# Performance work log

Hardware: AMD Instinct MI355X
Metric: run time of the kernel (lower is better)

## Reference

```python
import jax, jax.numpy as jnp
import numpy as np

N_V, N_E = 4096, 8192
ATOM_DIM, BOND_DIM_P1, H, N_LAYER = 64, 32, 128, 4


def _leaky(x):
    return jax.nn.leaky_relu(x, negative_slope=0.01)


def setup_inputs() -> dict:
    key = jax.random.key(0)
    ks = jax.random.split(key, 16)
    atom_ftr = jax.random.normal(ks[0], (N_V, ATOM_DIM), dtype=jnp.float32)
    bond_ftr = jax.random.normal(ks[1], (N_E, BOND_DIM_P1), dtype=jnp.float32)
    # one-hot incidence matrices: each edge column selects one source / one dest node
    src = jax.random.randint(ks[2], (N_E,), 0, N_V)
    dst = jax.random.randint(ks[3], (N_E,), 0, N_V)
    vew1 = jnp.zeros((N_V, N_E), jnp.float32).at[src, jnp.arange(N_E)].set(1.0)
    vew2 = jnp.zeros((N_V, N_E), jnp.float32).at[dst, jnp.arange(N_E)].set(1.0)
    def lin(k, o, i):
        s = 1.0 / np.sqrt(i)
        k1, k2 = jax.random.split(k)
        return (jax.random.uniform(k1, (o, i), jnp.float32, -s, s),
                jax.random.uniform(k2, (o,), jnp.float32, -s, s))
    vW1, vb1 = lin(ks[4], H, ATOM_DIM)
    vW2, vb2 = lin(ks[5], H, H)
    eW1, eb1 = lin(ks[6], H, BOND_DIM_P1)
    eW2, eb2 = lin(ks[7], H, H)
    mWs, mbs = [], []
    for l in range(N_LAYER):
        W, b = lin(ks[8 + l], H, H)
        mWs.append(W); mbs.append(b)
    return {
        'atom_ftr': atom_ftr, 'bond_ftr': bond_ftr, 'vew1': vew1, 'vew2': vew2,
        'vW1': vW1, 'vb1': vb1, 'vW2': vW2, 'vb2': vb2,
        'eW1': eW1, 'eb1': eb1, 'eW2': eW2, 'eb2': eb2,
        'mlp_W': jnp.stack(mWs), 'mlp_b': jnp.stack(mbs),
    }


def reference(atom_ftr, bond_ftr, vew1, vew2, vW1, vb1, vW2, vb2,
              eW1, eb1, eW2, eb2, mlp_W, mlp_b):
    # v_linear / e_linear: Linear -> leaky_relu -> Linear -> tanh (dropout p=0)
    hv = jnp.tanh(_leaky(atom_ftr @ vW1.T + vb1) @ vW2.T + vb2)   # [n_v, h]
    he = jnp.tanh(_leaky(bond_ftr @ eW1.T + eb1) @ eW2.T + eb2)   # [n_e, h]
    n_layer = mlp_W.shape[0]
    for l in range(n_layer):
        he_hv_2 = jax.nn.relu(he + vew2.T @ hv)       # [n_e, h]
        hv = hv + vew1 @ he_hv_2                      # [n_v, h]
        hv = _leaky(hv @ mlp_W[l].T + mlp_b[l])       # per-layer MLP (1 linear + leaky_relu)
    he_out = jnp.concatenate([vew1.T @ hv, vew2.T @ hv, he], axis=1)  # [n_e, 3h]
    return hv, he_out
```

## Files before the change

### kernel.cpp

```cpp
#include <hip/hip_runtime.h>
#include <hip/hip_bf16.h>

#define NV 4096
#define NE 8192
#define AD 64
#define BD 32
#define HD 128
#define NL 4
#define DEGCAP 32


__device__ __forceinline__ float leaky(float x) { return x > 0.f ? x : 0.01f * x; }
__device__ __forceinline__ int clampv(int x) { return min(max(x, 0), NV - 1); }

#define W_VW1T 0
#define W_VW2T 8192
#define W_EW1T 24576
#define W_EW2T 28672
#define W_MWT  45056
#define W_VB1  110592
#define W_VB2  110720
#define W_EB1  110848
#define W_EB2  110976
#define W_MB   111104
#define W_TOTAL 111616

#define OUT_HE 524288
#define ESTR   384

#define WS_SRC 0
#define WS_DST 32768
#define WS_DEG 65536
#define WS_ADJ 81920
#define WS_WB  606208
#define WS_HVA 1052672
#define WS_HVB 3149824

__global__ void prep_k(const float* __restrict__ vW1, const float* __restrict__ vW2,
                       const float* __restrict__ eW1, const float* __restrict__ eW2,
                       const float* __restrict__ mW,
                       const float* __restrict__ vb1, const float* __restrict__ vb2,
                       const float* __restrict__ eb1, const float* __restrict__ eb2,
                       const float* __restrict__ mb, float* __restrict__ wb,
                       int* __restrict__ deg) {
    int blk = blockIdx.x, t = threadIdx.x;
    if (blk < 436) {
        int i = blk * 256 + t;
        if (i >= W_TOTAL) return;
        float v;
        if (i < W_VW2T)      { int q = i;          int k = q / 128, j = q % 128; v = vW1[(long)j * AD + k]; }
        else if (i < W_EW1T) { int q = i - W_VW2T; int k = q / 128, j = q % 128; v = vW2[(long)j * HD + k]; }
        else if (i < W_EW2T) { int q = i - W_EW1T; int k = q / 128, j = q % 128; v = eW1[(long)j * BD + k]; }
        else if (i < W_MWT)  { int q = i - W_EW2T; int k = q / 128, j = q % 128; v = eW2[(long)j * HD + k]; }
        else if (i < W_VB1)  { int q = i - W_MWT;  int l = q / 16384, r = q % 16384;
                               int k = r / 128, j = r % 128;
                               v = mW[(long)l * 16384 + (long)j * HD + k]; }
        else if (i < W_VB2)  v = vb1[i - W_VB1];
        else if (i < W_EB1)  v = vb2[i - W_VB2];
        else if (i < W_EB2)  v = eb1[i - W_EB1];
        else if (i < W_MB)   v = eb2[i - W_EB2];
        else                 v = mb[i - W_MB];
        wb[i] = v;
    } else {
        int i = (blk - 436) * 256 + t;
        if (i < NV) deg[i] = 0;
    }
}

template<int K>
__device__ __forceinline__ float4 gemm_row(const float* __restrict__ xrow,
                                           const float* __restrict__ Wt, int jg) {
    float4 c = make_float4(0.f, 0.f, 0.f, 0.f);
    const float4* W4 = (const float4*)Wt;
#pragma unroll 8
    for (int k = 0; k < K; k += 4) {
        float4 xv = *(const float4*)(xrow + k);
        float4 w0 = W4[(k + 0) * 32 + jg];
        float4 w1 = W4[(k + 1) * 32 + jg];
        float4 w2 = W4[(k + 2) * 32 + jg];
        float4 w3 = W4[(k + 3) * 32 + jg];
        c.x = fmaf(xv.x, w0.x, fmaf(xv.y, w1.x, fmaf(xv.z, w2.x, fmaf(xv.w, w3.x, c.x))));
        c.y = fmaf(xv.x, w0.y, fmaf(xv.y, w1.y, fmaf(xv.z, w2.y, fmaf(xv.w, w3.y, c.y))));
        c.z = fmaf(xv.x, w0.z, fmaf(xv.y, w1.z, fmaf(xv.z, w2.z, fmaf(xv.w, w3.z, c.z))));
        c.w = fmaf(xv.x, w0.w, fmaf(xv.y, w1.w, fmaf(xv.z, w2.w, fmaf(xv.w, w3.w, c.w))));
    }
    return c;
}

__global__ __launch_bounds__(256, 3)
void fused_k(const uint4* __restrict__ vew1, const uint4* __restrict__ vew2,
             int* __restrict__ srcv, int* __restrict__ dstv,
             int* __restrict__ deg, int* __restrict__ adj,
             const float* __restrict__ atom, const float* __restrict__ bond,
             const float* __restrict__ wb,
             float* __restrict__ hv, float* __restrict__ outf) {
    __shared__ __align__(16) float xs[8 * AD];
    __shared__ __align__(16) float t1[8 * HD];
    int g = blockIdx.x, t = threadIdx.x;
    int grp = g / 7, rem = g % 7;
    if (rem < 4) {
        int blk = grp * 4 + rem;
        bool isv1 = (blk < 1024);
        const uint4* m = isv1 ? vew1 : vew2;
        int* out = isv1 ? srcv : dstv;
        int r0 = (blk & 1023) * 4;
        const uint4* p = m + (long)r0 * 2048;
#pragma unroll
        for (int b = 0; b < 2; b++) {
            uint4 u[16];
            unsigned o[16];
            int base = b * 4096 + t;
#pragma unroll
            for (int k = 0; k < 16; k++) u[k] = p[base + k * 256];
#pragma unroll
            for (int k = 0; k < 16; k++) o[k] = u[k].x | u[k].y | u[k].z | u[k].w;
            unsigned any = 0;
#pragma unroll
            for (int k = 0; k < 16; k++) any |= o[k];
            if (any == 0u) continue;
#pragma unroll
            for (int k = 0; k < 16; k++) {
                if (o[k] == 0u) continue;
                int i = base + k * 256;
                int row = r0 + (i >> 11);
                int col = (i << 2) & (NE - 1);
#pragma unroll
                for (int q = 0; q < 4; q++) {
                    unsigned val = (q == 0) ? u[k].x : (q == 1) ? u[k].y
                                 : (q == 2) ? u[k].z : u[k].w;
                    if (val) {
                        int e = col + q;
                        out[e] = row;
                        if (isv1) {
                            int pp = atomicAdd(&deg[row], 1);
                            if (pp < DEGCAP) adj[row * DEGCAP + pp] = e;
                        }
                    }
                }
            }
        }
    } else {
        int mu = grp * 3 + (rem - 4);
        int jg = t & 31, rg = t >> 5, j0 = jg * 4;
        if (mu < 512) {
            int r0 = mu * 8;
            for (int i = t; i < 8 * AD; i += 256) xs[i] = atom[(long)r0 * AD + i];
            __syncthreads();
            float4 c1 = gemm_row<AD>(xs + rg * AD, wb + W_VW1T, jg);
            float4 b1 = *(const float4*)(wb + W_VB1 + j0);
            c1.x = leaky(c1.x + b1.x); c1.y = leaky(c1.y + b1.y);
            c1.z = leaky(c1.z + b1.z); c1.w = leaky(c1.w + b1.w);
            *(float4*)(t1 + rg * HD + j0) = c1;
            __syncthreads();
            float4 c2 = gemm_row<HD>(t1 + rg * HD, wb + W_VW2T, jg);
            float4 b2 = *(const float4*)(wb + W_VB2 + j0);
            c2.x = tanhf(c2.x + b2.x); c2.y = tanhf(c2.y + b2.y);
            c2.z = tanhf(c2.z + b2.z); c2.w = tanhf(c2.w + b2.w);
            *(float4*)(hv + (long)(r0 + rg) * HD + j0) = c2;
        } else {
            int r0 = (mu - 512) * 8;
            if (t < 8 * BD) xs[t] = bond[(long)r0 * BD + t];
            __syncthreads();
            float4 c1 = gemm_row<BD>(xs + rg * BD, wb + W_EW1T, jg);
            float4 b1 = *(const float4*)(wb + W_EB1 + j0);
            c1.x = leaky(c1.x + b1.x); c1.y = leaky(c1.y + b1.y);
            c1.z = leaky(c1.z + b1.z); c1.w = leaky(c1.w + b1.w);
            *(float4*)(t1 + rg * HD + j0) = c1;
            __syncthreads();
            float4 c2 = gemm_row<HD>(t1 + rg * HD, wb + W_EW2T, jg);
            float4 b2 = *(const float4*)(wb + W_EB2 + j0);
            c2.x = tanhf(c2.x + b2.x); c2.y = tanhf(c2.y + b2.y);
            c2.z = tanhf(c2.z + b2.z); c2.w = tanhf(c2.w + b2.w);
            *(float4*)(outf + (long)OUT_HE + (long)(r0 + rg) * ESTR + 2 * HD + j0) = c2;
        }
    }
}

__global__ void layer_k(const float* __restrict__ hvin, const float* __restrict__ wb,
                        const int* __restrict__ deg, const int* __restrict__ adj,
                        const int* __restrict__ dstv, const float* __restrict__ outf,
                        float* __restrict__ hvout, int l, float* hv_out) {
    __shared__ __align__(16) float xs[4 * HD];
    int t = threadIdx.x, jg = t & 31, rg = t >> 5, j0 = jg * 4;
    int r = blockIdx.x * 4 + rg;
    float4 x = *(const float4*)(hvin + (long)r * HD + j0);
    int dn = min(deg[r], DEGCAP);
    const int* al = adj + r * DEGCAP;
    for (int i = 0; i < dn; i++) {
        int e = al[i]; e = max(0, min(e, NE - 1));
        int d = clampv(dstv[e]);
        float4 he = *(const float4*)(outf + (long)OUT_HE + (long)e * ESTR + 2 * HD + j0);
        float4 hd = *(const float4*)(hvin + (long)d * HD + j0);
        float s0 = he.x + hd.x, s1 = he.y + hd.y;
        float s2 = he.z + hd.z, s3 = he.w + hd.w;
        x.x += s0 > 0.f ? s0 : 0.f; x.y += s1 > 0.f ? s1 : 0.f;
        x.z += s2 > 0.f ? s2 : 0.f; x.w += s3 > 0.f ? s3 : 0.f;
    }
    *(float4*)(xs + rg * HD + j0) = x;
    __syncthreads();
    float4 c = gemm_row<HD>(xs + rg * HD, wb + W_MWT + l * 16384, jg);
    float4 b = *(const float4*)(wb + W_MB + l * HD + j0);
    c.x = leaky(c.x + b.x); c.y = leaky(c.y + b.y);
    c.z = leaky(c.z + b.z); c.w = leaky(c.w + b.w);
    long o = (long)r * HD + j0;
    *(float4*)(hvout + o) = c;
    if (hv_out) *(float4*)(hv_out + o) = c;
}

__global__ void out_he_k(const float* __restrict__ hv,
                         const int* __restrict__ src, const int* __restrict__ dst,
                         float* __restrict__ outf) {
    int e = blockIdx.x, t = threadIdx.x, j0 = t * 2;
    int s = clampv(src[e]), d = clampv(dst[e]);
    float2 a = *(const float2*)(hv + (long)s * HD + j0);
    float2 b = *(const float2*)(hv + (long)d * HD + j0);
    float* base = outf + (long)OUT_HE + (long)e * ESTR;
    *(float2*)(base + j0) = a;
    *(float2*)(base + HD + j0) = b;
}

extern "C" void kernel_launch(void* const* d_in, const int* in_sizes, int n_in,
                              void* d_out, int out_size, void* d_ws, size_t ws_size,
                              hipStream_t stream) {
    char* ws = (char*)d_ws;
    int*   srcv = (int*)(ws + WS_SRC);
    int*   dstv = (int*)(ws + WS_DST);
    int*   deg  = (int*)(ws + WS_DEG);
    int*   adj  = (int*)(ws + WS_ADJ);
    float* wb   = (float*)(ws + WS_WB);
    float* hvA  = (float*)(ws + WS_HVA);
    float* hvB  = (float*)(ws + WS_HVB);
    float* outf = (float*)d_out;

    prep_k<<<452, 256, 0, stream>>>(
        (const float*)d_in[4], (const float*)d_in[6], (const float*)d_in[8],
        (const float*)d_in[10], (const float*)d_in[12],
        (const float*)d_in[5], (const float*)d_in[7], (const float*)d_in[9],
        (const float*)d_in[11], (const float*)d_in[13], wb, deg);

    fused_k<<<3584, 256, 0, stream>>>(
        (const uint4*)d_in[2], (const uint4*)d_in[3], srcv, dstv, deg, adj,
        (const float*)d_in[0], (const float*)d_in[1], wb, hvA, outf);

    layer_k<<<NV / 4, 128, 0, stream>>>(hvA, wb, deg, adj, dstv, outf, hvB, 0, nullptr);
    layer_k<<<NV / 4, 128, 0, stream>>>(hvB, wb, deg, adj, dstv, outf, hvA, 1, nullptr);
    layer_k<<<NV / 4, 128, 0, stream>>>(hvA, wb, deg, adj, dstv, outf, hvB, 2, nullptr);
    layer_k<<<NV / 4, 128, 0, stream>>>(hvB, wb, deg, adj, dstv, outf, hvA, 3, outf);

    out_he_k<<<NE, 64, 0, stream>>>(hvA, srcv, dstv, outf);
}
```

Before: 410.6 us.

## Build dest adjacency and scatter edge outputs from last layer, use nontemporal loads

Builds a second per-node adjacency list for destination edges during the incidence scan, then has the final layer kernel scatter each node's result directly into the src/dst slices of the edge output. This removes the separate out_he kernel launch and its gather. It also switches the dense incidence matrix reads to nontemporal loads to avoid polluting cache. The cost is extra atomics for vew2 rows and serialized scatter loops per node in the last layer.

```diff
diff --git a/kernel.cpp b/kernel.cpp
--- a/kernel.cpp
+++ b/kernel.cpp
@@ -9,6 +9,8 @@
 #define NL 4
 #define DEGCAP 32
 
+
+typedef unsigned int v4u __attribute__((ext_vector_type(4)));
 
 __device__ __forceinline__ float leaky(float x) { return x > 0.f ? x : 0.01f * x; }
 __device__ __forceinline__ int clampv(int x) { return min(max(x, 0), NV - 1); }
@@ -28,13 +30,15 @@
 #define OUT_HE 524288
 #define ESTR   384
 
-#define WS_SRC 0
-#define WS_DST 32768
-#define WS_DEG 65536
-#define WS_ADJ 81920
-#define WS_WB  606208
-#define WS_HVA 1052672
-#define WS_HVB 3149824
+#define WS_SRC  0
+#define WS_DST  32768
+#define WS_DEGS 65536
+#define WS_ADJS 81920
+#define WS_DEGD 606208
+#define WS_ADJD 622592
+#define WS_WB   1146880
+#define WS_HVA  1593344
+#define WS_HVB  3690496
 
 __global__ void prep_k(const float* __restrict__ vW1, const float* __restrict__ vW2,
                        const float* __restrict__ eW1, const float* __restrict__ eW2,
@@ -42,7 +46,7 @@
                        const float* __restrict__ vb1, const float* __restrict__ vb2,
                        const float* __restrict__ eb1, const float* __restrict__ eb2,
                        const float* __restrict__ mb, float* __restrict__ wb,
-                       int* __restrict__ deg) {
+                       int* __restrict__ degS, int* __restrict__ degD) {
     int blk = blockIdx.x, t = threadIdx.x;
     if (blk < 436) {
         int i = blk * 256 + t;
@@ -63,7 +67,8 @@
         wb[i] = v;
     } else {
         int i = (blk - 436) * 256 + t;
-        if (i < NV) deg[i] = 0;
+        if (i < NV) degS[i] = 0;
+        else if (i < 2 * NV) degD[i - NV] = 0;
     }
 }
 
@@ -88,9 +93,10 @@
 }
 
 __global__ __launch_bounds__(256, 3)
-void fused_k(const uint4* __restrict__ vew1, const uint4* __restrict__ vew2,
+void fused_k(const v4u* __restrict__ vew1, const v4u* __restrict__ vew2,
              int* __restrict__ srcv, int* __restrict__ dstv,
-             int* __restrict__ deg, int* __restrict__ adj,
+             int* __restrict__ degS, int* __restrict__ adjS,
+             int* __restrict__ degD, int* __restrict__ adjD,
              const float* __restrict__ atom, const float* __restrict__ bond,
              const float* __restrict__ wb,
              float* __restrict__ hv, float* __restrict__ outf) {
@@ -101,17 +107,19 @@
     if (rem < 4) {
         int blk = grp * 4 + rem;
         bool isv1 = (blk < 1024);
-        const uint4* m = isv1 ? vew1 : vew2;
+        const v4u* m = isv1 ? vew1 : vew2;
         int* out = isv1 ? srcv : dstv;
+        int* deg = isv1 ? degS : degD;
+        int* adj = isv1 ? adjS : adjD;
         int r0 = (blk & 1023) * 4;
-        const uint4* p = m + (long)r0 * 2048;
+        const v4u* p = m + (long)r0 * 2048;
 #pragma unroll
         for (int b = 0; b < 2; b++) {
-            uint4 u[16];
+            v4u u[16];
             unsigned o[16];
             int base = b * 4096 + t;
 #pragma unroll
-            for (int k = 0; k < 16; k++) u[k] = p[base + k * 256];
+            for (int k = 0; k < 16; k++) u[k] = __builtin_nontemporal_load(&p[base + k * 256]);
 #pragma unroll
             for (int k = 0; k < 16; k++) o[k] = u[k].x | u[k].y | u[k].z | u[k].w;
             unsigned any = 0;
@@ -131,10 +139,8 @@
                     if (val) {
                         int e = col + q;
                         out[e] = row;
-                        if (isv1) {
-                            int pp = atomicAdd(&deg[row], 1);
-                            if (pp < DEGCAP) adj[row * DEGCAP + pp] = e;
-                        }
+                        int pp = atomicAdd(&deg[row], 1);
+                        if (pp < DEGCAP) adj[row * DEGCAP + pp] = e;
                     }
                 }
             }
@@ -177,17 +183,19 @@
 }
 
 __global__ void layer_k(const float* __restrict__ hvin, const float* __restrict__ wb,
-                        const int* __restrict__ deg, const int* __restrict__ adj,
+                        const int* __restrict__ degS, const int* __restrict__ adjS,
+                        const int* __restrict__ degD, const int* __restrict__ adjD,
                         const int* __restrict__ dstv, const float* __restrict__ outf,
-                        float* __restrict__ hvout, int l, float* hv_out) {
+                        float* __restrict__ hvout, int l, float* hv_out,
+                        float* __restrict__ outw) {
     __shared__ __align__(16) float xs[4 * HD];
     int t = threadIdx.x, jg = t & 31, rg = t >> 5, j0 = jg * 4;
     int r = blockIdx.x * 4 + rg;
     float4 x = *(const float4*)(hvin + (long)r * HD + j0);
-    int dn = min(deg[r], DEGCAP);
-    const int* al = adj + r * DEGCAP;
-    for (int i = 0; i < dn; i++) {
-        int e = al[i]; e = max(0, min(e, NE - 1));
+    int dnS = min(degS[r], DEGCAP);
+    const int* alS = adjS + r * DEGCAP;
+    for (int i = 0; i < dnS; i++) {
+        int e = alS[i]; e = max(0, min(e, NE - 1));
         int d = clampv(dstv[e]);
         float4 he = *(const float4*)(outf + (long)OUT_HE + (long)e * ESTR + 2 * HD + j0);
         float4 hd = *(const float4*)(hvin + (long)d * HD + j0);
@@ -204,19 +212,19 @@
     c.z = leaky(c.z + b.z); c.w = leaky(c.w + b.w);
     long o = (long)r * HD + j0;
     *(float4*)(hvout + o) = c;
-    if (hv_out) *(float4*)(hv_out + o) = c;
-}
-
-__global__ void out_he_k(const float* __restrict__ hv,
-                         const int* __restrict__ src, const int* __restrict__ dst,
-                         float* __restrict__ outf) {
-    int e = blockIdx.x, t = threadIdx.x, j0 = t * 2;
-    int s = clampv(src[e]), d = clampv(dst[e]);
-    float2 a = *(const float2*)(hv + (long)s * HD + j0);
-    float2 b = *(const float2*)(hv + (long)d * HD + j0);
-    float* base = outf + (long)OUT_HE + (long)e * ESTR;
-    *(float2*)(base + j0) = a;
-    *(float2*)(base + HD + j0) = b;
+    if (hv_out) {
+        *(float4*)(hv_out + o) = c;
+        for (int i = 0; i < dnS; i++) {
+            int e = alS[i]; e = max(0, min(e, NE - 1));
+            *(float4*)(outw + (long)OUT_HE + (long)e * ESTR + j0) = c;
+        }
+        int dnD = min(degD[r], DEGCAP);
+        const int* alD = adjD + r * DEGCAP;
+        for (int i = 0; i < dnD; i++) {
+            int e = alD[i]; e = max(0, min(e, NE - 1));
+            *(float4*)(outw + (long)OUT_HE + (long)e * ESTR + HD + j0) = c;
+        }
+    }
 }
 
 extern "C" void kernel_launch(void* const* d_in, const int* in_sizes, int n_in,
@@ -225,27 +233,28 @@
     char* ws = (char*)d_ws;
     int*   srcv = (int*)(ws + WS_SRC);
     int*   dstv = (int*)(ws + WS_DST);
-    int*   deg  = (int*)(ws + WS_DEG);
-    int*   adj  = (int*)(ws + WS_ADJ);
+    int*   degS = (int*)(ws + WS_DEGS);
+    int*   adjS = (int*)(ws + WS_ADJS);
+    int*   degD = (int*)(ws + WS_DEGD);
+    int*   adjD = (int*)(ws + WS_ADJD);
     float* wb   = (float*)(ws + WS_WB);
     float* hvA  = (float*)(ws + WS_HVA);
     float* hvB  = (float*)(ws + WS_HVB);
     float* outf = (float*)d_out;
 
-    prep_k<<<452, 256, 0, stream>>>(
+    prep_k<<<468, 256, 0, stream>>>(
         (const float*)d_in[4], (const float*)d_in[6], (const float*)d_in[8],
         (const float*)d_in[10], (const float*)d_in[12],
         (const float*)d_in[5], (const float*)d_in[7], (const float*)d_in[9],
-        (const float*)d_in[11], (const float*)d_in[13], wb, deg);
+        (const float*)d_in[11], (const float*)d_in[13], wb, degS, degD);
 
     fused_k<<<3584, 256, 0, stream>>>(
-        (const uint4*)d_in[2], (const uint4*)d_in[3], srcv, dstv, deg, adj,
+        (const v4u*)d_in[2], (const v4u*)d_in[3], srcv, dstv,
+        degS, adjS, degD, adjD,
         (const float*)d_in[0], (const float*)d_in[1], wb, hvA, outf);
 
-    layer_k<<<NV / 4, 128, 0, stream>>>(hvA, wb, deg, adj, dstv, outf, hvB, 0, nullptr);
-    layer_k<<<NV / 4, 128, 0, stream>>>(hvB, wb, deg, adj, dstv, outf, hvA, 1, nullptr);
-    layer_k<<<NV / 4, 128, 0, stream>>>(hvA, wb, deg, adj, dstv, outf, hvB, 2, nullptr);
-    layer_k<<<NV / 4, 128, 0, stream>>>(hvB, wb, deg, adj, dstv, outf, hvA, 3, outf);
-
-    out_he_k<<<NE, 64, 0, stream>>>(hvA, srcv, dstv, outf);
-}
+    layer_k<<<NV / 4, 128, 0, stream>>>(hvA, wb, degS, adjS, degD, adjD, dstv, outf, hvB, 0, nullptr, outf);
+    layer_k<<<NV / 4, 128, 0, stream>>>(hvB, wb, degS, adjS, degD, adjD, dstv, outf, hvA, 1, nullptr, outf);
+    layer_k<<<NV / 4, 128, 0, stream>>>(hvA, wb, degS, adjS, degD, adjD, dstv, outf, hvB, 2, nullptr, outf);
+    layer_k<<<NV / 4, 128, 0, stream>>>(hvB, wb, degS, adjS, degD, adjD, dstv, outf, hvA, 3, outf, outf);
+}
```

After: 369.3 us. 10.1% less time.
